# Kernel tuning notes

Measured on AMD Instinct MI355X. Metric: run time of the kernel, lower is better.

Reference implementation:

```python
import jax, jax.numpy as jnp
import numpy as np

NUM_HEADS = 16
DIM = 1024

def setup_inputs() -> dict:
    key = jax.random.key(0)
    ks = jax.random.split(key, 12)
    B, N, T, C = 4, 4096, 77, DIM
    s = 1.0 / np.sqrt(C)
    return {
        "hidden_states": jax.random.normal(ks[0], (B, N, C), jnp.float32),
        "encoder_hidden_states": jax.random.normal(ks[1], (B, T, C), jnp.float32),
        "attention_mask": jnp.zeros((B, N, T), jnp.float32),
        "Wq": jax.random.normal(ks[2], (C, C), jnp.float32) * s,
        "bq": jnp.zeros((C,), jnp.float32),
        "Wk": jax.random.normal(ks[3], (C, C), jnp.float32) * s,
        "bk": jnp.zeros((C,), jnp.float32),
        "Wv": jax.random.normal(ks[4], (C, C), jnp.float32) * s,
        "bv": jnp.zeros((C,), jnp.float32),
        "Wo": jax.random.normal(ks[5], (C, C), jnp.float32) * s,
        "bo": jnp.zeros((C,), jnp.float32),
    }

def reference(hidden_states, encoder_hidden_states, attention_mask,
              Wq, bq, Wk, bk, Wv, bv, Wo, bo):
    B, N, C = hidden_states.shape
    T = encoder_hidden_states.shape[1]
    H = NUM_HEADS
    D = C // H
    # QKV projections (torch Linear: x @ W.T + b)
    q = (hidden_states @ Wq.T + bq).reshape(B, N, H, D).transpose(0, 2, 1, 3)   # bhnd
    k = (encoder_hidden_states @ Wk.T + bk).reshape(B, T, H, D).transpose(0, 2, 1, 3)  # bhtd
    v = (encoder_hidden_states @ Wv.T + bv).reshape(B, T, H, D).transpose(0, 2, 1, 3)  # bhtd
    scale = 1.0 / jnp.sqrt(jnp.asarray(D, q.dtype))
    # scores [B,H,N,T]; additive mask broadcast over heads
    scores = jnp.einsum('bhnd,bhtd->bhnt', q, k) * scale + attention_mask[:, None, :, :]
    attn = jax.nn.softmax(scores, axis=-1)
    out = jnp.einsum('bhnt,bhtd->bhnd', attn, v)
    out = out.transpose(0, 2, 1, 3).reshape(B, N, C)
    return out @ Wo.T + bo
```

## Files before the change

kernel.cpp:

```cpp
#include <hip/hip_runtime.h>
#include <cstdint>

typedef __bf16 bf16x8 __attribute__((ext_vector_type(8)));
typedef float f32x4 __attribute__((ext_vector_type(4)));
typedef unsigned short u16;
typedef unsigned int u32;

__device__ __forceinline__ u16 f2bf(float f) {
    u32 u = __builtin_bit_cast(u32, f);
    u += 0x7fffu + ((u >> 16) & 1u);
    return (u16)(u >> 16);
}

__device__ __forceinline__ float bf2f(u32 x) {
    return __builtin_bit_cast(float, x << 16);
}

__device__ __forceinline__ void gl_lds16(const u16* g, u16* l) {
    __builtin_amdgcn_global_load_lds(
        (const __attribute__((address_space(1))) void*)g,
        (__attribute__((address_space(3))) void*)l,
        16, 0, 0);
}

__device__ __forceinline__ f32x4 mfma16(bf16x8 a, bf16x8 b, f32x4 c) {
    return __builtin_amdgcn_mfma_f32_16x16x32_bf16(a, b, c, 0, 0, 0);
}


struct CvtAll {
    const float* s[6];
    u16* d[6];
    int srcn[6];
    int totn[6];
    int off[6];
};

__global__ void cvt_all(CvtAll a) {
    const int blk = blockIdx.x;
    int seg = 0;
#pragma unroll
    for (int s = 1; s < 6; ++s) seg += (blk >= a.off[s]);
    const int i = ((blk - a.off[seg]) * 256 + threadIdx.x) * 4;
    if (i >= a.totn[seg]) return;
    float4 v = make_float4(0.f, 0.f, 0.f, 0.f);
    if (i < a.srcn[seg]) v = *(const float4*)&a.s[seg][i];
    ushort4 o;
    o.x = f2bf(v.x); o.y = f2bf(v.y); o.z = f2bf(v.z); o.w = f2bf(v.w);
    *(ushort4*)&a.d[seg][i] = o;
}

__device__ __forceinline__ void store_out(u16* C, long idx, float v) { C[idx] = f2bf(v); }
__device__ __forceinline__ void store_out(float* C, long idx, float v) { C[idx] = v; }

template <typename OutT, bool BA, bool BC>
__global__ __launch_bounds__(512, 2) void gemmP(
    const u16* __restrict__ A, const u16* __restrict__ W,
    const float* __restrict__ bias, OutT* __restrict__ C,
    int M, int N, int K) {
    __shared__ __align__(16) u16 As[3][256 * 32];
    __shared__ __align__(16) u16 Bs[3][128 * 32];

    const int tid = threadIdx.x;
    const int wid = tid >> 6, l = tid & 63;
    const int wr = wid >> 1, wc = wid & 1;
    const int l15 = l & 15, lg = l >> 4;

    const int lin = blockIdx.y * gridDim.x + blockIdx.x;
    const int cpx = (gridDim.x * gridDim.y) >> 3;
    const int swz = (lin & 7) * cpx + (lin >> 3);
    const long tn = swz & 7;
    const long tm = swz >> 3;

    const int srp = tid >> 3;
    const int sv = (tid & 7) ^ (srp & 7);
    const int sE = (sv >> 2) & 1;
    const int sKC = sv & 3;
    const long ar0 = tm * 256 + 2 * srp + sE;
    const long brow = tn * 128 + 2 * srp + sE;
    const long aRB = ar0 >> 2;
    const int aSub = (int)(ar0 & 3) * 16 + (sKC & 1) * 8;
    const int aCB = sKC >> 1;

    const int NT = K >> 5;

#define STAGE(s_, t_)                                                          \
    do {                                                                       \
        if (BA) {                                                              \
            const long cb_ = (long)((t_) * 2 + aCB) * (M >> 2);                \
            gl_lds16(A + (cb_ + aRB) * 64 + aSub, &As[s_][tid * 8]);           \
            gl_lds16(A + (cb_ + aRB + 32) * 64 + aSub,                         \
                     &As[s_][4096 + tid * 8]);                                 \
        } else {                                                               \
            gl_lds16(A + ar0 * (long)K + (t_) * 32 + sKC * 8,                  \
                     &As[s_][tid * 8]);                                        \
            gl_lds16(A + (ar0 + 128) * (long)K + (t_) * 32 + sKC * 8,          \
                     &As[s_][4096 + tid * 8]);                                 \
        }                                                                      \
        gl_lds16(W + brow * (long)K + (t_) * 32 + sKC * 8,                     \
                 &Bs[s_][tid * 8]);                                            \
    } while (0)

    const int e = l15 & 1;
    const int rphA = wr * 32 + (l15 >> 1);
    const int rphB = wc * 32 + (l15 >> 1);
    const int pA = ((e * 4 + lg) ^ (rphA & 7)) * 8;
    const int pB = ((e * 4 + lg) ^ (rphB & 7)) * 8;
    const int aOff = rphA * 64 + pA;
    const int bOff = rphB * 64 + pB;

    f32x4 acc[4][4] = {};

    STAGE(0, 0);
    STAGE(1, 1);

    for (int t = 0; t < NT; ++t) {
        if (t + 1 < NT)
            asm volatile("s_waitcnt vmcnt(3)" ::: "memory");
        else
            asm volatile("s_waitcnt vmcnt(0)" ::: "memory");
        __builtin_amdgcn_sched_barrier(0);
        __builtin_amdgcn_s_barrier();

        if (t + 2 < NT) {
            const int ns = (t + 2) % 3;
            STAGE(ns, t + 2);
        }

        const int c = t % 3;
        bf16x8 a[4], b[4];
#pragma unroll
        for (int nf = 0; nf < 4; ++nf)
            b[nf] = *(const bf16x8*)&Bs[c][bOff + nf * 512];
#pragma unroll
        for (int mf = 0; mf < 4; ++mf)
            a[mf] = *(const bf16x8*)&As[c][aOff + mf * 512];

        __builtin_amdgcn_s_setprio(1);
#pragma unroll
        for (int mf = 0; mf < 4; ++mf)
#pragma unroll
            for (int nf = 0; nf < 4; ++nf)
                acc[mf][nf] = mfma16(a[mf], b[nf], acc[mf][nf]);
        __builtin_amdgcn_s_setprio(0);
    }
#undef STAGE

    const long row0 = tm * 256 + wr * 64;
    const long col0 = tn * 128 + wc * 64;
    float bv[4];
#pragma unroll
    for (int nf = 0; nf < 4; ++nf) bv[nf] = bias[col0 + nf * 16 + l15];
    if (BC) {
        const long ct0 = col0 >> 4;
        const long rb = row0 >> 2;
#pragma unroll
        for (int mf = 0; mf < 4; ++mf)
#pragma unroll
            for (int nf = 0; nf < 4; ++nf)
#pragma unroll
                for (int r = 0; r < 4; ++r) {
                    const long idx =
                        ((ct0 + nf) * (long)(M >> 2) + rb + mf * 4 + lg) * 64 +
                        r * 16 + l15;
                    store_out(C, idx, acc[mf][nf][r] + bv[nf]);
                }
    } else {
#pragma unroll
        for (int mf = 0; mf < 4; ++mf)
#pragma unroll
            for (int nf = 0; nf < 4; ++nf)
#pragma unroll
                for (int r = 0; r < 4; ++r) {
                    const long row = row0 + mf * 16 + lg * 4 + r;
                    const long col = col0 + nf * 16 + l15;
                    store_out(C, row * N + col, acc[mf][nf][r] + bv[nf]);
                }
    }
}

template <bool VT>
__device__ __forceinline__ void gemm128_body(
    const u16* __restrict__ A, const u16* __restrict__ W,
    const float* __restrict__ bias, u16* __restrict__ C,
    int N, int K) {
    __shared__ __align__(16) u16 As[2][128 * 64];
    __shared__ __align__(16) u16 Bs[2][128 * 64];
    const int tid = threadIdx.x;
    const int w = tid >> 6, l = tid & 63;
    const int wr = w >> 1, wc = w & 1;
    const int l15 = l & 15, lg = l >> 4;
    const long tm = blockIdx.y, tn = blockIdx.x;
    const u16* Ab = A + tm * 128 * (long)K;
    const u16* Bb = W + tn * 128 * (long)K;

    const int srow = tid >> 3;
    const int skc = (tid & 7) ^ (srow & 7);

#define KV_STAGE(s_, k0_)                                                     \
    do {                                                                      \
        _Pragma("unroll")                                                     \
        for (int j_ = 0; j_ < 4; ++j_) {                                      \
            gl_lds16(Ab + (long)(srow + j_ * 32) * K + (k0_) + skc * 8,       \
                     &As[s_][j_ * 2048 + tid * 8]);                           \
            gl_lds16(Bb + (long)(srow + j_ * 32) * K + (k0_) + skc * 8,       \
                     &Bs[s_][j_ * 2048 + tid * 8]);                           \
        }                                                                     \
    } while (0)

    f32x4 acc[4][4] = {};
    const int NT = K >> 6;

    KV_STAGE(0, 0);
    __syncthreads();

    for (int t = 0; t < NT; ++t) {
        const int c = t & 1;
        if (t + 1 < NT) KV_STAGE(c ^ 1, (t + 1) << 6);

#pragma unroll
        for (int kk = 0; kk < 2; ++kk) {
            bf16x8 a[4], bb[4];
#pragma unroll
            for (int m = 0; m < 4; ++m) {
                const int ar = wr * 64 + m * 16 + l15;
                const int cc = (kk * 4 + lg) ^ (ar & 7);
                a[m] = *(const bf16x8*)&As[c][ar * 64 + cc * 8];
            }
#pragma unroll
            for (int n = 0; n < 4; ++n) {
                const int br = wc * 64 + n * 16 + l15;
                const int cc = (kk * 4 + lg) ^ (br & 7);
                bb[n] = *(const bf16x8*)&Bs[c][br * 64 + cc * 8];
            }
#pragma unroll
            for (int m = 0; m < 4; ++m)
#pragma unroll
                for (int n = 0; n < 4; ++n)
                    acc[m][n] = mfma16(a[m], bb[n], acc[m][n]);
        }
        __syncthreads();
    }
#undef KV_STAGE

    const long row0 = tm * 128 + wr * 64;
    const long col0 = tn * 128 + wc * 64;
#pragma unroll
    for (int m = 0; m < 4; ++m)
#pragma unroll
        for (int n = 0; n < 4; ++n)
#pragma unroll
            for (int r = 0; r < 4; ++r) {
                const float v = acc[m][n][r] + bias[col0 + n * 16 + l15];
                if (VT) {
                    const int row = (int)(row0 + m * 16 + lg * 4 + r);
                    if (row < 308) {
                        const int bb = row / 77;
                        const int t = row - bb * 77;
                        const int ch = (int)(col0 + n * 16 + l15);
                        const long idx = (long)bb * 98304 +
                                         ((long)(t >> 4) * 256 + (ch >> 2)) * 64 +
                                         (ch & 3) * 16 + (t & 15);
                        C[idx] = f2bf(v);
                    }
                } else {
                    const long idx = (((col0 >> 4) + n) * 96L + (row0 >> 2) + m * 4 + lg) * 64 +
                                     r * 16 + l15;
                    C[idx] = f2bf(v);
                }
            }
}

__global__ __launch_bounds__(256) void gemm_kv(
    const u16* __restrict__ A,
    const u16* __restrict__ Wk, const float* __restrict__ bk, u16* __restrict__ Ko,
    const u16* __restrict__ Wv, const float* __restrict__ bv, u16* __restrict__ Vo,
    int N, int K) {
    if (blockIdx.z == 0)
        gemm128_body<false>(A, Wk, bk, Ko, N, K);
    else
        gemm128_body<true>(A, Wv, bv, Vo, N, K);
}

__global__ __launch_bounds__(256, 3) void attn_fused(
    const u16* __restrict__ Q,
    const u16* __restrict__ Kb,
    const u16* __restrict__ Vt,
    const float* __restrict__ mask,
    u16* __restrict__ Ao) {
    __shared__ u16 Ps[128 * 104];
    __shared__ u16 Ms[128 * 88];

    const int h = blockIdx.x, b = blockIdx.y, nt = blockIdx.z;
    const int tid = threadIdx.x;
    const int w = tid >> 6, l = tid & 63;
    const int l15 = l & 15, lg = l >> 4;

    {
        const float* mb = mask + ((long)b * 4096 + nt * 128) * 77;
        const int lane = tid & 63;
        const int rg = tid >> 6;
#pragma unroll
        for (int g = 0; g < 32; ++g) {
            const int row = g * 4 + rg;
            const long rb = (long)row * 77;
            Ms[row * 88 + lane] = f2bf(mb[rb + lane]);
            const int t2 = lane + 64;
            if (t2 < 80) {
                const float v1 = (t2 < 77) ? mb[rb + t2] : -1e38f;
                Ms[row * 88 + t2] = f2bf(v1);
            }
        }
    }
    __syncthreads();

    const int qrow = b * 4096 + nt * 128 + w * 32;

    f32x4 acc[5][2] = {};
#pragma unroll
    for (int kk = 0; kk < 64; kk += 32) {
        const int d = kk + lg * 8;
        const int cb = h * 4 + (d >> 4);
        const int dlow = d & 15;
        bf16x8 kf[5], qf[2];
#pragma unroll
        for (int n = 0; n < 5; ++n) {
            const int row = b * 77 + n * 16 + l15;
            kf[n] = *(const bf16x8*)&Kb[((long)cb * 96 + (row >> 2)) * 64 +
                                        (row & 3) * 16 + dlow];
        }
#pragma unroll
        for (int m = 0; m < 2; ++m) {
            const int row = qrow + m * 16 + l15;
            qf[m] = *(const bf16x8*)&Q[((long)cb * 4096 + (row >> 2)) * 64 +
                                       (row & 3) * 16 + dlow];
        }
#pragma unroll
        for (int n = 0; n < 5; ++n)
#pragma unroll
            for (int m = 0; m < 2; ++m)
                acc[n][m] = mfma16(kf[n], qf[m], acc[n][m]);
    }

#pragma unroll
    for (int m = 0; m < 2; ++m) {
        const int lrow = w * 32 + m * 16 + l15;
        float vals[5][4];
        float rmax = -3e38f;
#pragma unroll
        for (int n = 0; n < 5; ++n) {
            const uint2 mm = *(const uint2*)&Ms[lrow * 88 + n * 16 + lg * 4];
            const float mv0 = bf2f(mm.x & 0xffffu);
            const float mv1 = bf2f(mm.x >> 16);
            const float mv2 = bf2f(mm.y & 0xffffu);
            const float mv3 = bf2f(mm.y >> 16);
            vals[n][0] = fmaf(acc[n][m][0], 0.125f, mv0);
            vals[n][1] = fmaf(acc[n][m][1], 0.125f, mv1);
            vals[n][2] = fmaf(acc[n][m][2], 0.125f, mv2);
            vals[n][3] = fmaf(acc[n][m][3], 0.125f, mv3);
#pragma unroll
            for (int r = 0; r < 4; ++r) rmax = fmaxf(rmax, vals[n][r]);
        }
        rmax = fmaxf(rmax, __shfl_xor(rmax, 16, 64));
        rmax = fmaxf(rmax, __shfl_xor(rmax, 32, 64));
        float s = 0.f;
#pragma unroll
        for (int n = 0; n < 5; ++n)
#pragma unroll
            for (int r = 0; r < 4; ++r) {
                const float e = __expf(vals[n][r] - rmax);
                vals[n][r] = e;
                s += e;
            }
        s += __shfl_xor(s, 16, 64);
        s += __shfl_xor(s, 32, 64);
        const float inv = 1.f / s;
#pragma unroll
        for (int n = 0; n < 5; ++n) {
            const u32 lo = (u32)f2bf(vals[n][0] * inv) |
                           ((u32)f2bf(vals[n][1] * inv) << 16);
            const u32 hi = (u32)f2bf(vals[n][2] * inv) |
                           ((u32)f2bf(vals[n][3] * inv) << 16);
            *(uint2*)&Ps[(w * 32 + m * 16 + l15) * 104 + n * 16 + lg * 4] =
                make_uint2(lo, hi);
        }
        *(uint2*)&Ps[(w * 32 + m * 16 + l15) * 104 + 80 + lg * 4] = make_uint2(0, 0);
    }

    f32x4 o[2][4] = {};
#pragma unroll
    for (int kt = 0; kt < 96; kt += 32) {
        bf16x8 pa[2], vf[4];
#pragma unroll
        for (int m = 0; m < 2; ++m)
            pa[m] = *(const bf16x8*)&Ps[(w * 32 + m * 16 + l15) * 104 + kt + lg * 8];
        const int t0 = kt + lg * 8;
#pragma unroll
        for (int n = 0; n < 4; ++n) {
            const int ch = h * 64 + n * 16 + l15;
            vf[n] = *(const bf16x8*)&Vt[(long)b * 98304 +
                                        ((long)(t0 >> 4) * 256 + (ch >> 2)) * 64 +
                                        (ch & 3) * 16 + (t0 & 15)];
        }
#pragma unroll
        for (int m = 0; m < 2; ++m)
#pragma unroll
            for (int n = 0; n < 4; ++n)
                o[m][n] = mfma16(pa[m], vf[n], o[m][n]);
    }

#pragma unroll
    for (int m = 0; m < 2; ++m)
#pragma unroll
        for (int n = 0; n < 4; ++n)
#pragma unroll
            for (int r = 0; r < 4; ++r) {
                const long idx = ((long)(h * 4 + n) * 4096 +
                                  b * 1024 + nt * 32 + w * 8 + m * 4 + lg) * 64 +
                                 r * 16 + l15;
                Ao[idx] = f2bf(o[m][n][r]);
            }
}

extern "C" void kernel_launch(void* const* d_in, const int* in_sizes, int n_in,
                              void* d_out, int out_size, void* d_ws, size_t ws_size,
                              hipStream_t stream) {
    const float* hidden = (const float*)d_in[0];
    const float* enc = (const float*)d_in[1];
    const float* mask = (const float*)d_in[2];
    const float* Wq = (const float*)d_in[3];
    const float* bq = (const float*)d_in[4];
    const float* Wk = (const float*)d_in[5];
    const float* bk = (const float*)d_in[6];
    const float* Wv = (const float*)d_in[7];
    const float* bv = (const float*)d_in[8];
    const float* Wo = (const float*)d_in[9];
    const float* bo = (const float*)d_in[10];
    float* out = (float*)d_out;

    char* ws = (char*)d_ws;
    u16* hiddenB = (u16*)(ws);
    u16* Qb = (u16*)(ws + 33554432L);
    u16* AoB = (u16*)(ws + 2 * 33554432L);
    u16* WqB = (u16*)(ws + 3 * 33554432L);
    u16* WkB = WqB + 1048576;
    u16* WvB = WkB + 1048576;
    u16* WoB = WvB + 1048576;
    u16* encB = WoB + 1048576;
    u16* Kbuf = encB + 393216;
    u16* VtBuf = Kbuf + 393216;

    CvtAll ca;
    ca.s[0] = hidden; ca.d[0] = hiddenB; ca.srcn[0] = 16777216; ca.totn[0] = 16777216;
    ca.s[1] = Wq;  ca.d[1] = WqB; ca.srcn[1] = 1048576; ca.totn[1] = 1048576;
    ca.s[2] = Wk;  ca.d[2] = WkB; ca.srcn[2] = 1048576; ca.totn[2] = 1048576;
    ca.s[3] = Wv;  ca.d[3] = WvB; ca.srcn[3] = 1048576; ca.totn[3] = 1048576;
    ca.s[4] = Wo;  ca.d[4] = WoB; ca.srcn[4] = 1048576; ca.totn[4] = 1048576;
    ca.s[5] = enc; ca.d[5] = encB; ca.srcn[5] = 315392; ca.totn[5] = 393216;
    ca.off[0] = 0;
    ca.off[1] = 16384;
    ca.off[2] = 17408;
    ca.off[3] = 18432;
    ca.off[4] = 19456;
    ca.off[5] = 20480;
    cvt_all<<<dim3(20864), 256, 0, stream>>>(ca);

    gemmP<u16, false, true><<<dim3(8, 64), 512, 0, stream>>>(
        hiddenB, WqB, bq, Qb, 16384, 1024, 1024);
    gemm_kv<<<dim3(8, 3, 2), 256, 0, stream>>>(encB, WkB, bk, Kbuf, WvB, bv, VtBuf, 1024, 1024);

    attn_fused<<<dim3(16, 4, 32), 256, 0, stream>>>(Qb, Kbuf, VtBuf, mask, AoB);

    gemmP<float, true, false><<<dim3(8, 64), 512, 0, stream>>>(
        AoB, WoB, bo, out, 16384, 1024, 1024);
}
```

Before: 199.6 us.

## Precompute padded bf16 mask once instead of per-head staging in LDS

Adds a separate kernel that converts the fp32 [B,N,77] additive mask into a padded bf16 [B*N,80] buffer, done once rather than once per head in each attention block. The attention kernel then reads mask values directly from global memory, drops the Ms LDS array and its __syncthreads, and raises launch bounds to 4 blocks per CU. This removes 16x redundant fp32 mask reads and the LDS staging cost. In exchange it adds an extra launch and uncoalesced 8-byte global loads inside the softmax.

```diff
diff --git a/kernel.cpp b/kernel.cpp
--- a/kernel.cpp
+++ b/kernel.cpp
@@ -48,6 +48,21 @@
     ushort4 o;
     o.x = f2bf(v.x); o.y = f2bf(v.y); o.z = f2bf(v.z); o.w = f2bf(v.w);
     *(ushort4*)&a.d[seg][i] = o;
+}
+
+__global__ void cvt_mask(const float* __restrict__ mask, u16* __restrict__ maskB) {
+    const int j = (blockIdx.x * 256 + threadIdx.x) * 4;
+    if (j >= 1310720) return;
+    const int row = j / 80;
+    const int t0 = j - row * 80;
+    const long src = (long)row * 77 + t0;
+    const u16 pad = f2bf(-1e38f);
+    ushort4 o;
+    o.x = f2bf(mask[src]);
+    o.y = (t0 + 1 < 77) ? f2bf(mask[src + 1]) : pad;
+    o.z = (t0 + 2 < 77) ? f2bf(mask[src + 2]) : pad;
+    o.w = (t0 + 3 < 77) ? f2bf(mask[src + 3]) : pad;
+    *(ushort4*)&maskB[j] = o;
 }
 
 __device__ __forceinline__ void store_out(u16* C, long idx, float v) { C[idx] = f2bf(v); }
@@ -282,37 +297,18 @@
         gemm128_body<true>(A, Wv, bv, Vo, N, K);
 }
 
-__global__ __launch_bounds__(256, 3) void attn_fused(
+__global__ __launch_bounds__(256, 4) void attn_fused(
     const u16* __restrict__ Q,
     const u16* __restrict__ Kb,
     const u16* __restrict__ Vt,
-    const float* __restrict__ mask,
+    const u16* __restrict__ maskB,
     u16* __restrict__ Ao) {
     __shared__ u16 Ps[128 * 104];
-    __shared__ u16 Ms[128 * 88];
 
     const int h = blockIdx.x, b = blockIdx.y, nt = blockIdx.z;
     const int tid = threadIdx.x;
     const int w = tid >> 6, l = tid & 63;
     const int l15 = l & 15, lg = l >> 4;
-
-    {
-        const float* mb = mask + ((long)b * 4096 + nt * 128) * 77;
-        const int lane = tid & 63;
-        const int rg = tid >> 6;
-#pragma unroll
-        for (int g = 0; g < 32; ++g) {
-            const int row = g * 4 + rg;
-            const long rb = (long)row * 77;
-            Ms[row * 88 + lane] = f2bf(mb[rb + lane]);
-            const int t2 = lane + 64;
-            if (t2 < 80) {
-                const float v1 = (t2 < 77) ? mb[rb + t2] : -1e38f;
-                Ms[row * 88 + t2] = f2bf(v1);
-            }
-        }
-    }
-    __syncthreads();
 
     const int qrow = b * 4096 + nt * 128 + w * 32;
 
@@ -344,20 +340,16 @@
 
 #pragma unroll
     for (int m = 0; m < 2; ++m) {
-        const int lrow = w * 32 + m * 16 + l15;
+        const long mrow = ((long)qrow + m * 16 + l15) * 80;
         float vals[5][4];
         float rmax = -3e38f;
 #pragma unroll
         for (int n = 0; n < 5; ++n) {
-            const uint2 mm = *(const uint2*)&Ms[lrow * 88 + n * 16 + lg * 4];
-            const float mv0 = bf2f(mm.x & 0xffffu);
-            const float mv1 = bf2f(mm.x >> 16);
-            const float mv2 = bf2f(mm.y & 0xffffu);
-            const float mv3 = bf2f(mm.y >> 16);
-            vals[n][0] = fmaf(acc[n][m][0], 0.125f, mv0);
-            vals[n][1] = fmaf(acc[n][m][1], 0.125f, mv1);
-            vals[n][2] = fmaf(acc[n][m][2], 0.125f, mv2);
-            vals[n][3] = fmaf(acc[n][m][3], 0.125f, mv3);
+            const uint2 mm = *(const uint2*)&maskB[mrow + n * 16 + lg * 4];
+            vals[n][0] = fmaf(acc[n][m][0], 0.125f, bf2f(mm.x & 0xffffu));
+            vals[n][1] = fmaf(acc[n][m][1], 0.125f, bf2f(mm.x >> 16));
+            vals[n][2] = fmaf(acc[n][m][2], 0.125f, bf2f(mm.y & 0xffffu));
+            vals[n][3] = fmaf(acc[n][m][3], 0.125f, bf2f(mm.y >> 16));
 #pragma unroll
             for (int r = 0; r < 4; ++r) rmax = fmaxf(rmax, vals[n][r]);
         }
@@ -449,6 +441,7 @@
     u16* encB = WoB + 1048576;
     u16* Kbuf = encB + 393216;
     u16* VtBuf = Kbuf + 393216;
+    u16* maskBuf = VtBuf + 393216;
 
     CvtAll ca;
     ca.s[0] = hidden; ca.d[0] = hiddenB; ca.srcn[0] = 16777216; ca.totn[0] = 16777216;
@@ -464,12 +457,13 @@
     ca.off[4] = 19456;
     ca.off[5] = 20480;
     cvt_all<<<dim3(20864), 256, 0, stream>>>(ca);
+    cvt_mask<<<dim3(1280), 256, 0, stream>>>(mask, maskBuf);
 
     gemmP<u16, false, true><<<dim3(8, 64), 512, 0, stream>>>(
         hiddenB, WqB, bq, Qb, 16384, 1024, 1024);
     gemm_kv<<<dim3(8, 3, 2), 256, 0, stream>>>(encB, WkB, bk, Kbuf, WvB, bv, VtBuf, 1024, 1024);
 
-    attn_fused<<<dim3(16, 4, 32), 256, 0, stream>>>(Qb, Kbuf, VtBuf, mask, AoB);
+    attn_fused<<<dim3(16, 4, 32), 256, 0, stream>>>(Qb, Kbuf, VtBuf, maskBuf, AoB);
 
     gemmP<float, true, false><<<dim3(8, 64), 512, 0, stream>>>(
         AoB, WoB, bo, out, 16384, 1024, 1024);
```

After: 161.4 us. 1.24x faster.
